# Optimization experiments

Hardware: AMD Instinct MI355X
Metric: run time of the kernel (lower is better)

Reference implementation:

```python
import jax, jax.numpy as jnp
import numpy as np

B, S, HID, H = 4, 2048, 768, 12
D = HID // H  # 64
SCALE = 1.0 / (D ** 0.5)


def setup_inputs() -> dict:
    key = jax.random.key(0)
    ks = jax.random.split(key, 12)
    std = 0.02
    inp = {
        'Q': jax.random.normal(ks[0], (B, S, HID), jnp.float32),
        'K': jax.random.normal(ks[1], (B, S, HID), jnp.float32),
        'V': jax.random.normal(ks[2], (B, S, HID), jnp.float32),
        'attn_mask': jax.random.randint(ks[3], (B, S, S), 0, 2) == 1,
        'Wq': jax.random.normal(ks[4], (HID, HID), jnp.float32) * std,
        'bq': jnp.zeros((HID,), jnp.float32),
        'Wk': jax.random.normal(ks[5], (HID, HID), jnp.float32) * std,
        'bk': jnp.zeros((HID,), jnp.float32),
        'Wv': jax.random.normal(ks[6], (HID, HID), jnp.float32) * std,
        'bv': jnp.zeros((HID,), jnp.float32),
        'Wo': jax.random.normal(ks[7], (HID, HID), jnp.float32) * std,
        'bo': jnp.zeros((HID,), jnp.float32),
    }
    return inp


def reference(Q, K, V, attn_mask, Wq, bq, Wk, bk, Wv, bv, Wo, bo):
    b, s, _ = Q.shape
    # projections -> [b, h, s, d]
    def split_heads(x):
        return x.reshape(b, s, H, D).transpose(0, 2, 1, 3)
    q = split_heads(Q @ Wq + bq)
    k = split_heads(K @ Wk + bk)
    v = split_heads(V @ Wv + bv)
    # eager attention: materialize full [b,h,s,s] scores
    scores = jnp.einsum('bhqd,bhkd->bhqk', q, k) * SCALE
    scores = jnp.where(attn_mask[:, None, :, :], jnp.float32(-1e9), scores)
    attn_prob = jax.nn.softmax(scores, axis=-1)
    # dropout is identity in eval mode
    context = jnp.einsum('bhqk,bhkd->bhqd', attn_prob, v)
    context = context.transpose(0, 2, 1, 3).reshape(b, s, H * D)
    output = context @ Wo + bo
    return (output, attn_prob)
```

## Files before the change

kernel.cpp:

```cpp
#include <hip/hip_runtime.h>
#include <hip/hip_bf16.h>
#include <stdint.h>

#define BB 4
#define SS 2048
#define HIDD 768
#define HH 12
#define DD 64
#define SCALE_F 0.125f

using bf16 = __hip_bfloat16;
typedef __attribute__((ext_vector_type(8))) short short8v;
typedef __attribute__((ext_vector_type(4))) float f32x4;

__device__ __forceinline__ float ldf(const float* p, size_t i) { return p[i]; }
__device__ __forceinline__ float ldf(const bf16* p, size_t i) { return __bfloat162float(p[i]); }
__device__ __forceinline__ void stf(float* p, size_t i, float v) { p[i] = v; }
__device__ __forceinline__ void stf(bf16* p, size_t i, float v) { p[i] = __float2bfloat16(v); }

__device__ __forceinline__ uint32_t bfb(float f) {
    bf16 h = __float2bfloat16(f);
    uint16_t u;
    __builtin_memcpy(&u, &h, 2);
    return (uint32_t)u;
}
__device__ __forceinline__ float b2f(uint32_t u) {
    uint32_t w = u << 16;
    float f;
    __builtin_memcpy(&f, &w, 4);
    return f;
}

__device__ __forceinline__ uint4 load8p(const bf16* p) { return *(const uint4*)p; }
__device__ __forceinline__ uint4 load8p(const float* p) {
    float4 a = *(const float4*)p;
    float4 b = *(const float4*)(p + 4);
    uint4 r;
    r.x = bfb(a.x) | (bfb(a.y) << 16);
    r.y = bfb(a.z) | (bfb(a.w) << 16);
    r.z = bfb(b.x) | (bfb(b.y) << 16);
    r.w = bfb(b.z) | (bfb(b.w) << 16);
    return r;
}

template <int ITERS, typename TIN>
__device__ __forceinline__ void stage_tile(char* dst, const TIN* src, int rowStride, int tid) {
    #pragma unroll
    for (int i = 0; i < ITERS; i++) {
        int u = tid + (i << 8);
        int r = u >> 3, sg = u & 7;
        uint4 v = load8p(src + (size_t)r * rowStride + sg * 8);
        *(uint4*)(dst + r * 128 + ((sg * 16) ^ ((r & 7) << 4))) = v;
    }
}

__device__ __forceinline__ short8v ldfrag(const char* base, int row, int bofs) {
    return *(const short8v*)(base + row * 128 + (bofs ^ ((row & 7) << 4)));
}

__global__ void detect_kernel(const uint32_t* __restrict__ qraw,
                              const uint32_t* __restrict__ mraw,
                              int* __restrict__ flags) {
    __shared__ int ci, cn;
    int tid = threadIdx.x;
    if (tid == 0) { ci = 0; cn = 0; }
    __syncthreads();
    int li = 0;
    for (int l = 0; l < 8; l++) {
        uint32_t w = qraw[tid + l * 256];
        #pragma unroll
        for (int h = 0; h < 2; h++) {
            uint32_t bits = (h ? (w >> 16) : (w & 0xffffu)) << 16;
            float f = __uint_as_float(bits);
            float a = fabsf(f);
            if (a != 0.0f && (a > 1e3f || a < 1e-4f)) li++;
        }
    }
    int ln = 0;
    for (int l = 0; l < 4; l++) {
        if (mraw[tid + l * 256] > 1u) ln++;
    }
    atomicAdd(&ci, li);
    atomicAdd(&cn, ln);
    __syncthreads();
    if (tid == 0) {
        flags[0] = (ci > 1024) ? 0 : 1;
        flags[1] = (cn > 64) ? 1 : 0;
    }
}

__global__ __launch_bounds__(256) void bitpack_mask(const int* __restrict__ flags,
                                                    const void* __restrict__ maskp,
                                                    uint64_t* __restrict__ mbits) {
    int gw = (int)((blockIdx.x * 256 + threadIdx.x) >> 6);
    int lane = threadIdx.x & 63;
    int byteM = flags[1];
    const int* mi = (const int*)maskp;
    const uint8_t* mb = (const uint8_t*)maskp;
    for (int it = 0; it < 64; it++) {
        size_t wi = (size_t)gw * 64 + it;
        size_t e = wi * 64 + lane;
        int m = byteM ? (int)mb[e] : mi[e];
        unsigned long long b = __ballot(m != 0);
        if (lane == 0) mbits[wi] = (uint64_t)b;
    }
}

template <typename T>
__global__ __launch_bounds__(256) void transpose_w(const int* __restrict__ flags, int want,
                                                   const T* __restrict__ W0,
                                                   const T* __restrict__ W1,
                                                   const T* __restrict__ W2,
                                                   const T* __restrict__ W3,
                                                   bf16* __restrict__ WT) {
    if (flags[0] != want) return;
    __shared__ uint16_t tb[64][65];
    int tid = threadIdx.x;
    int z = blockIdx.z;
    const T* W = (z == 0) ? W0 : (z == 1) ? W1 : (z == 2) ? W2 : W3;
    int k0 = blockIdx.y * 64, n0 = blockIdx.x * 64;
    #pragma unroll
    for (int l = 0; l < 16; l++) {
        int idx = tid + l * 256;
        int r = idx >> 6, c = idx & 63;
        tb[c][r] = (uint16_t)bfb(ldf(W, (size_t)(k0 + r) * HIDD + n0 + c));
    }
    __syncthreads();
    bf16* dst = WT + (size_t)z * HIDD * HIDD;
    #pragma unroll
    for (int l = 0; l < 16; l++) {
        int idx = tid + l * 256;
        int r = idx >> 6, c = idx & 63;
        *(uint16_t*)&dst[(size_t)(n0 + r) * HIDD + k0 + c] = tb[r][c];
    }
}

template <typename TX, typename TO, int HSPLIT>
__global__ __launch_bounds__(256) void gemm2(const int* __restrict__ flags, int want,
                                             const TX* __restrict__ X,
                                             const bf16* __restrict__ WT,
                                             const TO* __restrict__ bias,
                                             bf16* __restrict__ Yh,
                                             TO* __restrict__ Yl) {
    if (flags[0] != want) return;
    __shared__ char xs[128 * 128];
    __shared__ char ws[64 * 128];
    int tid = threadIdx.x;
    int lane = tid & 63, w = tid >> 6;
    int g = lane >> 4, t = lane & 15;
    int row0 = blockIdx.y * 128, n0 = blockIdx.x * 64;
    const f32x4 fz = {0.f, 0.f, 0.f, 0.f};
    f32x4 acc[2][4];
    #pragma unroll
    for (int rb = 0; rb < 2; rb++)
        #pragma unroll
        for (int c = 0; c < 4; c++) acc[rb][c] = fz;
    for (int kt = 0; kt < HIDD; kt += 64) {
        stage_tile<4>(xs, X + (size_t)row0 * HIDD + kt, HIDD, tid);
        stage_tile<2>(ws, WT + (size_t)n0 * HIDD + kt, HIDD, tid);
        __syncthreads();
        #pragma unroll
        for (int ks = 0; ks < 2; ks++) {
            short8v a0 = ldfrag(xs, w * 32 + t, g * 16 + ks * 64);
            short8v a1 = ldfrag(xs, w * 32 + 16 + t, g * 16 + ks * 64);
            #pragma unroll
            for (int c = 0; c < 4; c++) {
                short8v b = ldfrag(ws, c * 16 + t, g * 16 + ks * 64);
                acc[0][c] = __builtin_amdgcn_mfma_f32_16x16x32_bf16(a0, b, acc[0][c], 0, 0, 0);
                acc[1][c] = __builtin_amdgcn_mfma_f32_16x16x32_bf16(a1, b, acc[1][c], 0, 0, 0);
            }
        }
        __syncthreads();
    }
    #pragma unroll
    for (int c = 0; c < 4; c++) {
        int col = n0 + c * 16 + t;
        float bv = ldf(bias, (size_t)col);
        #pragma unroll
        for (int rb = 0; rb < 2; rb++) {
            #pragma unroll
            for (int r = 0; r < 4; r++) {
                int row = row0 + w * 32 + rb * 16 + g * 4 + r;
                float v = acc[rb][c][r] + bv;
                if (HSPLIT) {
                    int b_ = row >> 11, s = row & 2047, h = col >> 6, d = col & 63;
                    Yh[(((size_t)b_ * HH + h) * SS + s) * DD + d] = __float2bfloat16(v);
                } else {
                    stf(Yl, (size_t)row * HIDD + col, v);
                }
            }
        }
    }
}

__global__ __launch_bounds__(256) void transpose_v(const bf16* __restrict__ vh,
                                                   bf16* __restrict__ vt) {
    __shared__ uint16_t tb[64][65];
    int tid = threadIdx.x;
    int s0 = blockIdx.x * 64, bh = blockIdx.y;
    const bf16* src = vh + ((size_t)bh * SS + s0) * DD;
    #pragma unroll
    for (int i = 0; i < 2; i++) {
        int u = tid + (i << 8);
        int r = u >> 3, sg = u & 7;
        uint4 v = *(const uint4*)(src + (size_t)r * DD + sg * 8);
        uint32_t wv[4] = {v.x, v.y, v.z, v.w};
        #pragma unroll
        for (int j = 0; j < 4; j++) {
            tb[r][sg * 8 + 2 * j]     = (uint16_t)(wv[j] & 0xffffu);
            tb[r][sg * 8 + 2 * j + 1] = (uint16_t)(wv[j] >> 16);
        }
    }
    __syncthreads();
    bf16* dst = vt + (size_t)bh * DD * SS + s0;
    #pragma unroll
    for (int i = 0; i < 2; i++) {
        int u = tid + (i << 8);
        int d = u >> 3, sg = u & 7;
        uint32_t w0 = (uint32_t)tb[sg * 8 + 0][d] | ((uint32_t)tb[sg * 8 + 1][d] << 16);
        uint32_t w1 = (uint32_t)tb[sg * 8 + 2][d] | ((uint32_t)tb[sg * 8 + 3][d] << 16);
        uint32_t w2 = (uint32_t)tb[sg * 8 + 4][d] | ((uint32_t)tb[sg * 8 + 5][d] << 16);
        uint32_t w3 = (uint32_t)tb[sg * 8 + 6][d] | ((uint32_t)tb[sg * 8 + 7][d] << 16);
        uint4 o; o.x = w0; o.y = w1; o.z = w2; o.w = w3;
        *(uint4*)(dst + (size_t)d * SS + sg * 8) = o;
    }
}

template <typename T>
__global__ __launch_bounds__(256) void fused_attn2(const int* __restrict__ flags, int want,
                                                   const bf16* __restrict__ qh,
                                                   const bf16* __restrict__ kh,
                                                   const bf16* __restrict__ vt,
                                                   const uint64_t* __restrict__ mbits,
                                                   T* __restrict__ P,
                                                   bf16* __restrict__ ctx) {
    if (flags[0] != want) return;
    __shared__ char pl[16 * 4096];
    __shared__ char st[64 * 128];
    __shared__ float red[4][16];
    __shared__ float invl[16];
    int tid = threadIdx.x;
    int lane = tid & 63, w = tid >> 6;
    int g = lane >> 4, t = lane & 15;
    int q0 = blockIdx.x * 16, bh = blockIdx.y;
    int b_ = bh / HH, h = bh - b_ * HH;
    const f32x4 fz = {0.f, 0.f, 0.f, 0.f};

    const bf16* qbase = qh + ((size_t)bh * SS + q0 + t) * DD;
    short8v aq[2];
    aq[0] = *(const short8v*)(qbase + g * 8);
    aq[1] = *(const short8v*)(qbase + 32 + g * 8);

    const bf16* kbh = kh + (size_t)bh * SS * DD;
    const bf16* vbh = vt + (size_t)bh * DD * SS;
    size_t mrow[4];
    #pragma unroll
    for (int r = 0; r < 4; r++) mrow[r] = ((size_t)b_ * SS + q0 + g * 4 + r) * (SS / 64);

    float sum4[4] = {0.f, 0.f, 0.f, 0.f};
    int bitIdx = w * 16 + t;

    for (int kt = 0; kt < SS; kt += 64) {
        stage_tile<2>(st, kbh + (size_t)kt * DD, DD, tid);
        __syncthreads();
        f32x4 s = fz;
        #pragma unroll
        for (int ks = 0; ks < 2; ks++) {
            short8v b = ldfrag(st, w * 16 + t, g * 16 + ks * 64);
            s = __builtin_amdgcn_mfma_f32_16x16x32_bf16(aq[ks], b, s, 0, 0, 0);
        }
        #pragma unroll
        for (int r = 0; r < 4; r++) {
            uint64_t mw = mbits[mrow[r] + (kt >> 6)];
            int msk = (int)((mw >> bitIdx) & 1ull);
            float sv = msk ? -1e30f : s[r] * SCALE_F;
            float p = __expf(fminf(sv, 30.0f));
            sum4[r] += p;
            int row = g * 4 + r;
            int colb = (kt + w * 16 + t) * 2;
            *(uint16_t*)(pl + row * 4096 + (colb ^ ((row & 7) << 4))) = (uint16_t)bfb(p);
        }
        __syncthreads();
    }
    #pragma unroll
    for (int r = 0; r < 4; r++) {
        float v = sum4[r];
        #pragma unroll
        for (int d = 1; d < 16; d <<= 1) v += __shfl_xor(v, d);
        if (t == 0) red[w][g * 4 + r] = v;
    }
    __syncthreads();
    if (tid < 16) {
        float tot = red[0][tid] + red[1][tid] + red[2][tid] + red[3][tid];
        invl[tid] = (tot > 0.f) ? 1.0f / tot : 0.0f;
    }
    __syncthreads();
    float invr[4];
    #pragma unroll
    for (int r = 0; r < 4; r++) invr[r] = invl[g * 4 + r];
    int prow = tid >> 4;
    float pinv = invl[prow];
    T* Prow = P + ((size_t)bh * SS + q0 + prow) * SS;

    f32x4 o = fz;
    for (int kt = 0; kt < SS; kt += 64) {
        stage_tile<2>(st, vbh + kt, SS, tid);
        __syncthreads();
        #pragma unroll
        for (int ks = 0; ks < 2; ks++) {
            short8v ap = *(const short8v*)(pl + t * 4096 +
                            (((kt + ks * 32 + g * 8) * 2) ^ ((t & 7) << 4)));
            short8v bv = ldfrag(st, w * 16 + t, g * 16 + ks * 64);
            o = __builtin_amdgcn_mfma_f32_16x16x32_bf16(ap, bv, o, 0, 0, 0);
        }
        {
            int col = kt + (tid & 15) * 4;
            uint2 pv2 = *(const uint2*)(pl + prow * 4096 + ((col * 2) ^ ((prow & 7) << 4)));
            float p0 = b2f(pv2.x & 0xffffu) * pinv;
            float p1 = b2f(pv2.x >> 16) * pinv;
            float p2 = b2f(pv2.y & 0xffffu) * pinv;
            float p3 = b2f(pv2.y >> 16) * pinv;
            stf(Prow, (size_t)col + 0, p0);
            stf(Prow, (size_t)col + 1, p1);
            stf(Prow, (size_t)col + 2, p2);
            stf(Prow, (size_t)col + 3, p3);
        }
        __syncthreads();
    }
    #pragma unroll
    for (int r = 0; r < 4; r++) {
        int q = q0 + g * 4 + r;
        ctx[((size_t)b_ * SS + q) * HIDD + h * DD + w * 16 + t] =
            __float2bfloat16(o[r] * invr[r]);
    }
}

extern "C" void kernel_launch(void* const* d_in, const int* in_sizes, int n_in,
                              void* d_out, int out_size, void* d_ws, size_t ws_size,
                              hipStream_t stream) {
    const size_t nqkv = (size_t)BB * SS * HIDD;
    const size_t nw = (size_t)HIDD * HIDD;
    const size_t nmw = (size_t)BB * SS * (SS / 64);

    bf16* qh = (bf16*)d_ws;
    bf16* kh = qh + nqkv;
    bf16* vh = kh + nqkv;
    bf16* vt = vh + nqkv;
    bf16* WT = vt + nqkv;
    uint64_t* mbits = (uint64_t*)(WT + 4 * nw);
    int* flags = (int*)(mbits + nmw);
    bf16* ctx = vh;

    detect_kernel<<<1, 256, 0, stream>>>((const uint32_t*)d_in[0], (const uint32_t*)d_in[3], flags);
    bitpack_mask<<<1024, 256, 0, stream>>>(flags, d_in[3], mbits);

    dim3 blk(256);
    dim3 gW(HIDD / 64, HIDD / 64, 4);
    dim3 gG(HIDD / 64, (BB * SS) / 128);
    dim3 gT(SS / 64, BB * HH);
    dim3 gF(SS / 16, BB * HH);

    transpose_w<float><<<gW, blk, 0, stream>>>(flags, 0,
        (const float*)d_in[4], (const float*)d_in[6], (const float*)d_in[8],
        (const float*)d_in[10], WT);
    transpose_w<bf16><<<gW, blk, 0, stream>>>(flags, 1,
        (const bf16*)d_in[4], (const bf16*)d_in[6], (const bf16*)d_in[8],
        (const bf16*)d_in[10], WT);

    {
        gemm2<float, float, 1><<<gG, blk, 0, stream>>>(flags, 0, (const float*)d_in[0],
            WT + 0 * nw, (const float*)d_in[5], qh, (float*)nullptr);
        gemm2<float, float, 1><<<gG, blk, 0, stream>>>(flags, 0, (const float*)d_in[1],
            WT + 1 * nw, (const float*)d_in[7], kh, (float*)nullptr);
        gemm2<float, float, 1><<<gG, blk, 0, stream>>>(flags, 0, (const float*)d_in[2],
            WT + 2 * nw, (const float*)d_in[9], vh, (float*)nullptr);
        gemm2<bf16, bf16, 1><<<gG, blk, 0, stream>>>(flags, 1, (const bf16*)d_in[0],
            WT + 0 * nw, (const bf16*)d_in[5], qh, (bf16*)nullptr);
        gemm2<bf16, bf16, 1><<<gG, blk, 0, stream>>>(flags, 1, (const bf16*)d_in[1],
            WT + 1 * nw, (const bf16*)d_in[7], kh, (bf16*)nullptr);
        gemm2<bf16, bf16, 1><<<gG, blk, 0, stream>>>(flags, 1, (const bf16*)d_in[2],
            WT + 2 * nw, (const bf16*)d_in[9], vh, (bf16*)nullptr);
    }

    transpose_v<<<gT, blk, 0, stream>>>(vh, vt);

    {
        float* out = (float*)d_out;
        float* P = out + nqkv;
        fused_attn2<float><<<gF, blk, 0, stream>>>(flags, 0, qh, kh, vt, mbits, P, ctx);
    }
    {
        bf16* out = (bf16*)d_out;
        bf16* P = out + nqkv;
        fused_attn2<bf16><<<gF, blk, 0, stream>>>(flags, 1, qh, kh, vt, mbits, P, ctx);
    }

    {
        float* out = (float*)d_out;
        gemm2<bf16, float, 0><<<gG, blk, 0, stream>>>(flags, 0, ctx, WT + 3 * nw,
            (const float*)d_in[11], (bf16*)nullptr, out);
    }
    {
        bf16* out = (bf16*)d_out;
        gemm2<bf16, bf16, 0><<<gG, blk, 0, stream>>>(flags, 1, ctx, WT + 3 * nw,
            (const bf16*)d_in[11], (bf16*)nullptr, out);
    }
}
```

Before: 1.705 ms.

## Restructure attention to single pass with register-prefetched K/V and direct-to-LDS GEMM loads

The fused attention kernel now computes scores and P·V in one loop, reading K and V fragments straight from global memory into registers with one-tile-ahead prefetch. This removes the separate K/V LDS staging passes and most barriers. The probability matrix is written at the end with wide non-temporal stores. Inputs and biases are pre-converted to bf16 and f32 in staging kernels (using the P output region as scratch), and the GEMM uses global_load_lds to copy tiles directly into LDS. Duplicate flag-gated launches are collapsed into one runtime-branching kernel each, at the cost of extra conversion passes and reuse of output memory as temporary space.

```diff
diff --git a/kernel.cpp b/kernel.cpp
--- a/kernel.cpp
+++ b/kernel.cpp
@@ -8,15 +8,18 @@
 #define HH 12
 #define DD 64
 #define SCALE_F 0.125f
+#define NQKV ((size_t)BB * SS * HIDD)
+#define NW ((size_t)HIDD * HIDD)
+#define NMW ((size_t)BB * SS * (SS / 64))
 
 using bf16 = __hip_bfloat16;
 typedef __attribute__((ext_vector_type(8))) short short8v;
 typedef __attribute__((ext_vector_type(4))) float f32x4;
+typedef __attribute__((ext_vector_type(4))) float fvec4;
+typedef __attribute__((ext_vector_type(4))) unsigned int uvec4;
 
 __device__ __forceinline__ float ldf(const float* p, size_t i) { return p[i]; }
 __device__ __forceinline__ float ldf(const bf16* p, size_t i) { return __bfloat162float(p[i]); }
-__device__ __forceinline__ void stf(float* p, size_t i, float v) { p[i] = v; }
-__device__ __forceinline__ void stf(bf16* p, size_t i, float v) { p[i] = __float2bfloat16(v); }
 
 __device__ __forceinline__ uint32_t bfb(float f) {
     bf16 h = __float2bfloat16(f);
@@ -30,8 +33,6 @@
     __builtin_memcpy(&f, &w, 4);
     return f;
 }
-
-__device__ __forceinline__ uint4 load8p(const bf16* p) { return *(const uint4*)p; }
 __device__ __forceinline__ uint4 load8p(const float* p) {
     float4 a = *(const float4*)p;
     float4 b = *(const float4*)(p + 4);
@@ -43,19 +44,14 @@
     return r;
 }
 
-template <int ITERS, typename TIN>
-__device__ __forceinline__ void stage_tile(char* dst, const TIN* src, int rowStride, int tid) {
-    #pragma unroll
-    for (int i = 0; i < ITERS; i++) {
-        int u = tid + (i << 8);
-        int r = u >> 3, sg = u & 7;
-        uint4 v = load8p(src + (size_t)r * rowStride + sg * 8);
-        *(uint4*)(dst + r * 128 + ((sg * 16) ^ ((r & 7) << 4))) = v;
-    }
-}
-
 __device__ __forceinline__ short8v ldfrag(const char* base, int row, int bofs) {
     return *(const short8v*)(base + row * 128 + (bofs ^ ((row & 7) << 4)));
+}
+
+typedef __attribute__((address_space(1))) void as1_void;
+typedef __attribute__((address_space(3))) void as3_void;
+__device__ __forceinline__ void gload16(const void* g, void* l) {
+    __builtin_amdgcn_global_load_lds((as1_void*)g, (as3_void*)l, 16, 0, 0);
 }
 
 __global__ void detect_kernel(const uint32_t* __restrict__ qraw,
@@ -106,27 +102,56 @@
     }
 }
 
-template <typename T>
-__global__ __launch_bounds__(256) void transpose_w(const int* __restrict__ flags, int want,
-                                                   const T* __restrict__ W0,
-                                                   const T* __restrict__ W1,
-                                                   const T* __restrict__ W2,
-                                                   const T* __restrict__ W3,
-                                                   bf16* __restrict__ WT) {
-    if (flags[0] != want) return;
+__global__ __launch_bounds__(256) void convert_in(const int* __restrict__ flags,
+                                                  const void* __restrict__ Q,
+                                                  const void* __restrict__ K,
+                                                  const void* __restrict__ V,
+                                                  bf16* __restrict__ xb) {
+    int isbf = flags[0];
+    int z = blockIdx.y;
+    const void* src = (z == 0) ? Q : (z == 1) ? K : V;
+    size_t base = ((size_t)blockIdx.x * 256 + threadIdx.x) * 8;
+    bf16* dst = xb + (size_t)z * NQKV + base;
+    if (isbf) {
+        *(uint4*)dst = *(const uint4*)((const bf16*)src + base);
+    } else {
+        *(uint4*)dst = load8p((const float*)src + base);
+    }
+}
+
+__global__ void convert_bias(const int* __restrict__ flags,
+                             const void* __restrict__ b0, const void* __restrict__ b1,
+                             const void* __restrict__ b2, const void* __restrict__ b3,
+                             float* __restrict__ bf) {
+    int isbf = flags[0];
+    for (int i = threadIdx.x; i < 4 * HIDD; i += 256) {
+        int z = i / HIDD, j = i - z * HIDD;
+        const void* b = (z == 0) ? b0 : (z == 1) ? b1 : (z == 2) ? b2 : b3;
+        bf[i] = isbf ? b2f((uint32_t) * ((const uint16_t*)b + j)) : ((const float*)b)[j];
+    }
+}
+
+__global__ __launch_bounds__(256) void transpose_w2(const int* __restrict__ flags,
+                                                    const void* __restrict__ W0,
+                                                    const void* __restrict__ W1,
+                                                    const void* __restrict__ W2,
+                                                    const void* __restrict__ W3,
+                                                    bf16* __restrict__ WT) {
+    int isbf = flags[0];
     __shared__ uint16_t tb[64][65];
     int tid = threadIdx.x;
     int z = blockIdx.z;
-    const T* W = (z == 0) ? W0 : (z == 1) ? W1 : (z == 2) ? W2 : W3;
+    const void* W = (z == 0) ? W0 : (z == 1) ? W1 : (z == 2) ? W2 : W3;
     int k0 = blockIdx.y * 64, n0 = blockIdx.x * 64;
     #pragma unroll
     for (int l = 0; l < 16; l++) {
         int idx = tid + l * 256;
         int r = idx >> 6, c = idx & 63;
-        tb[c][r] = (uint16_t)bfb(ldf(W, (size_t)(k0 + r) * HIDD + n0 + c));
-    }
-    __syncthreads();
-    bf16* dst = WT + (size_t)z * HIDD * HIDD;
+        size_t off = (size_t)(k0 + r) * HIDD + n0 + c;
+        tb[c][r] = isbf ? *((const uint16_t*)W + off) : (uint16_t)bfb(((const float*)W)[off]);
+    }
+    __syncthreads();
+    bf16* dst = WT + (size_t)z * NW;
     #pragma unroll
     for (int l = 0; l < 16; l++) {
         int idx = tid + l * 256;
@@ -135,14 +160,14 @@
     }
 }
 
-template <typename TX, typename TO, int HSPLIT>
-__global__ __launch_bounds__(256) void gemm2(const int* __restrict__ flags, int want,
-                                             const TX* __restrict__ X,
+template <int HSPLIT>
+__global__ __launch_bounds__(256) void gemm3(const int* __restrict__ flags,
+                                             const bf16* __restrict__ X,
                                              const bf16* __restrict__ WT,
-                                             const TO* __restrict__ bias,
+                                             const float* __restrict__ biasf,
                                              bf16* __restrict__ Yh,
-                                             TO* __restrict__ Yl) {
-    if (flags[0] != want) return;
+                                             float* __restrict__ Yf,
+                                             bf16* __restrict__ Yb) {
     __shared__ char xs[128 * 128];
     __shared__ char ws[64 * 128];
     int tid = threadIdx.x;
@@ -155,9 +180,22 @@
     for (int rb = 0; rb < 2; rb++)
         #pragma unroll
         for (int c = 0; c < 4; c++) acc[rb][c] = fz;
+    int r8 = tid >> 3, c8 = tid & 7;
+    const char* Xb0 = (const char*)(X + (size_t)row0 * HIDD);
+    const char* Wb0 = (const char*)(WT + (size_t)n0 * HIDD);
     for (int kt = 0; kt < HIDD; kt += 64) {
-        stage_tile<4>(xs, X + (size_t)row0 * HIDD + kt, HIDD, tid);
-        stage_tile<2>(ws, WT + (size_t)n0 * HIDD + kt, HIDD, tid);
+        #pragma unroll
+        for (int i = 0; i < 4; i++) {
+            int r = r8 + i * 32;
+            gload16(Xb0 + (size_t)r * (HIDD * 2) + kt * 2 + ((c8 * 16) ^ ((r & 7) << 4)),
+                    xs + w * 1024 + i * 4096);
+        }
+        #pragma unroll
+        for (int i = 0; i < 2; i++) {
+            int r = r8 + i * 32;
+            gload16(Wb0 + (size_t)r * (HIDD * 2) + kt * 2 + ((c8 * 16) ^ ((r & 7) << 4)),
+                    ws + w * 1024 + i * 4096);
+        }
         __syncthreads();
         #pragma unroll
         for (int ks = 0; ks < 2; ks++) {
@@ -172,10 +210,11 @@
         }
         __syncthreads();
     }
+    int isbf = flags[0];
     #pragma unroll
     for (int c = 0; c < 4; c++) {
         int col = n0 + c * 16 + t;
-        float bv = ldf(bias, (size_t)col);
+        float bv = biasf[col];
         #pragma unroll
         for (int rb = 0; rb < 2; rb++) {
             #pragma unroll
@@ -183,10 +222,11 @@
                 int row = row0 + w * 32 + rb * 16 + g * 4 + r;
                 float v = acc[rb][c][r] + bv;
                 if (HSPLIT) {
-                    int b_ = row >> 11, s = row & 2047, h = col >> 6, d = col & 63;
-                    Yh[(((size_t)b_ * HH + h) * SS + s) * DD + d] = __float2bfloat16(v);
+                    int b_ = row >> 11, s = row & 2047, h2 = col >> 6, d = col & 63;
+                    Yh[(((size_t)b_ * HH + h2) * SS + s) * DD + d] = __float2bfloat16(v);
                 } else {
-                    stf(Yl, (size_t)row * HIDD + col, v);
+                    if (isbf) Yb[(size_t)row * HIDD + col] = __float2bfloat16(v);
+                    else      Yf[(size_t)row * HIDD + col] = v;
                 }
             }
         }
@@ -226,17 +266,16 @@
     }
 }
 
-template <typename T>
-__global__ __launch_bounds__(256) void fused_attn2(const int* __restrict__ flags, int want,
+__global__ __launch_bounds__(256) void fused_attn3(const int* __restrict__ flags,
                                                    const bf16* __restrict__ qh,
                                                    const bf16* __restrict__ kh,
                                                    const bf16* __restrict__ vt,
                                                    const uint64_t* __restrict__ mbits,
-                                                   T* __restrict__ P,
+                                                   float* __restrict__ Pf,
+                                                   bf16* __restrict__ Ph,
                                                    bf16* __restrict__ ctx) {
-    if (flags[0] != want) return;
+    const int isf32 = (flags[0] == 0);
     __shared__ char pl[16 * 4096];
-    __shared__ char st[64 * 128];
     __shared__ float red[4][16];
     __shared__ float invl[16];
     int tid = threadIdx.x;
@@ -245,43 +284,73 @@
     int q0 = blockIdx.x * 16, bh = blockIdx.y;
     int b_ = bh / HH, h = bh - b_ * HH;
     const f32x4 fz = {0.f, 0.f, 0.f, 0.f};
+    int bitIdx = w * 16 + t;
 
     const bf16* qbase = qh + ((size_t)bh * SS + q0 + t) * DD;
-    short8v aq[2];
-    aq[0] = *(const short8v*)(qbase + g * 8);
-    aq[1] = *(const short8v*)(qbase + 32 + g * 8);
-
-    const bf16* kbh = kh + (size_t)bh * SS * DD;
-    const bf16* vbh = vt + (size_t)bh * DD * SS;
-    size_t mrow[4];
-    #pragma unroll
-    for (int r = 0; r < 4; r++) mrow[r] = ((size_t)b_ * SS + q0 + g * 4 + r) * (SS / 64);
+    short8v aq0 = *(const short8v*)(qbase + g * 8);
+    short8v aq1 = *(const short8v*)(qbase + 32 + g * 8);
+
+    const bf16* kcol = kh + ((size_t)bh * SS + bitIdx) * DD + g * 8;
+    const bf16* vrow = vt + ((size_t)bh * DD + bitIdx) * SS + g * 8;
+    const uint64_t* mrowp[4];
+    #pragma unroll
+    for (int r = 0; r < 4; r++)
+        mrowp[r] = mbits + ((size_t)b_ * SS + q0 + g * 4 + r) * (SS / 64);
+
+    short8v cK0 = *(const short8v*)(kcol);
+    short8v cK1 = *(const short8v*)(kcol + 32);
+    short8v cV0 = *(const short8v*)(vrow);
+    short8v cV1 = *(const short8v*)(vrow + 32);
+    uint64_t cM[4];
+    #pragma unroll
+    for (int r = 0; r < 4; r++) cM[r] = mrowp[r][0];
 
     float sum4[4] = {0.f, 0.f, 0.f, 0.f};
-    int bitIdx = w * 16 + t;
+    f32x4 o = fz;
 
     for (int kt = 0; kt < SS; kt += 64) {
-        stage_tile<2>(st, kbh + (size_t)kt * DD, DD, tid);
-        __syncthreads();
+        int ktn = (kt + 64) & (SS - 1);
+        const bf16* kn = kcol + (size_t)ktn * DD;
+        const bf16* vn = vrow + ktn;
+        short8v nK0 = *(const short8v*)(kn);
+        short8v nK1 = *(const short8v*)(kn + 32);
+        short8v nV0 = *(const short8v*)(vn);
+        short8v nV1 = *(const short8v*)(vn + 32);
+        int wn = ((kt >> 6) + 1) & 31;
+        uint64_t nM[4];
+        #pragma unroll
+        for (int r = 0; r < 4; r++) nM[r] = mrowp[r][wn];
+
         f32x4 s = fz;
-        #pragma unroll
-        for (int ks = 0; ks < 2; ks++) {
-            short8v b = ldfrag(st, w * 16 + t, g * 16 + ks * 64);
-            s = __builtin_amdgcn_mfma_f32_16x16x32_bf16(aq[ks], b, s, 0, 0, 0);
-        }
+        s = __builtin_amdgcn_mfma_f32_16x16x32_bf16(aq0, cK0, s, 0, 0, 0);
+        s = __builtin_amdgcn_mfma_f32_16x16x32_bf16(aq1, cK1, s, 0, 0, 0);
+
         #pragma unroll
         for (int r = 0; r < 4; r++) {
-            uint64_t mw = mbits[mrow[r] + (kt >> 6)];
-            int msk = (int)((mw >> bitIdx) & 1ull);
+            int msk = (int)((cM[r] >> bitIdx) & 1ull);
             float sv = msk ? -1e30f : s[r] * SCALE_F;
             float p = __expf(fminf(sv, 30.0f));
             sum4[r] += p;
             int row = g * 4 + r;
-            int colb = (kt + w * 16 + t) * 2;
+            int colb = (kt + bitIdx) * 2;
             *(uint16_t*)(pl + row * 4096 + (colb ^ ((row & 7) << 4))) = (uint16_t)bfb(p);
         }
-        __syncthreads();
-    }
+
+        asm volatile("s_waitcnt lgkmcnt(0)" ::: "memory");
+        __builtin_amdgcn_s_barrier();
+        asm volatile("" ::: "memory");
+        __builtin_amdgcn_sched_barrier(0);
+
+        short8v ap0 = *(const short8v*)(pl + t * 4096 + (((kt + g * 8) * 2) ^ ((t & 7) << 4)));
+        short8v ap1 = *(const short8v*)(pl + t * 4096 + (((kt + 32 + g * 8) * 2) ^ ((t & 7) << 4)));
+        o = __builtin_amdgcn_mfma_f32_16x16x32_bf16(ap0, cV0, o, 0, 0, 0);
+        o = __builtin_amdgcn_mfma_f32_16x16x32_bf16(ap1, cV1, o, 0, 0, 0);
+
+        cK0 = nK0; cK1 = nK1; cV0 = nV0; cV1 = nV1;
+        #pragma unroll
+        for (int r = 0; r < 4; r++) cM[r] = nM[r];
+    }
+
     #pragma unroll
     for (int r = 0; r < 4; r++) {
         float v = sum4[r];
@@ -295,114 +364,83 @@
         invl[tid] = (tot > 0.f) ? 1.0f / tot : 0.0f;
     }
     __syncthreads();
-    float invr[4];
-    #pragma unroll
-    for (int r = 0; r < 4; r++) invr[r] = invl[g * 4 + r];
-    int prow = tid >> 4;
-    float pinv = invl[prow];
-    T* Prow = P + ((size_t)bh * SS + q0 + prow) * SS;
-
-    f32x4 o = fz;
-    for (int kt = 0; kt < SS; kt += 64) {
-        stage_tile<2>(st, vbh + kt, SS, tid);
-        __syncthreads();
-        #pragma unroll
-        for (int ks = 0; ks < 2; ks++) {
-            short8v ap = *(const short8v*)(pl + t * 4096 +
-                            (((kt + ks * 32 + g * 8) * 2) ^ ((t & 7) << 4)));
-            short8v bv = ldfrag(st, w * 16 + t, g * 16 + ks * 64);
-            o = __builtin_amdgcn_mfma_f32_16x16x32_bf16(ap, bv, o, 0, 0, 0);
-        }
-        {
-            int col = kt + (tid & 15) * 4;
-            uint2 pv2 = *(const uint2*)(pl + prow * 4096 + ((col * 2) ^ ((prow & 7) << 4)));
-            float p0 = b2f(pv2.x & 0xffffu) * pinv;
-            float p1 = b2f(pv2.x >> 16) * pinv;
-            float p2 = b2f(pv2.y & 0xffffu) * pinv;
-            float p3 = b2f(pv2.y >> 16) * pinv;
-            stf(Prow, (size_t)col + 0, p0);
-            stf(Prow, (size_t)col + 1, p1);
-            stf(Prow, (size_t)col + 2, p2);
-            stf(Prow, (size_t)col + 3, p3);
-        }
-        __syncthreads();
-    }
+
     #pragma unroll
     for (int r = 0; r < 4; r++) {
         int q = q0 + g * 4 + r;
-        ctx[((size_t)b_ * SS + q) * HIDD + h * DD + w * 16 + t] =
-            __float2bfloat16(o[r] * invr[r]);
+        ctx[((size_t)b_ * SS + q) * HIDD + h * DD + bitIdx] =
+            __float2bfloat16(o[r] * invl[g * 4 + r]);
+    }
+
+    int prow = tid >> 4, cg = tid & 15;
+    float pinv = invl[prow];
+    size_t rowb = ((size_t)bh * SS + q0 + prow) * SS;
+    if (isf32) {
+        #pragma unroll
+        for (int c0 = 0; c0 < SS; c0 += 128) {
+            int col = c0 + cg * 8;
+            uint4 pv = *(const uint4*)(pl + prow * 4096 + ((col * 2) ^ ((prow & 7) << 4)));
+            fvec4 lo = {b2f(pv.x & 0xffffu) * pinv, b2f(pv.x >> 16) * pinv,
+                        b2f(pv.y & 0xffffu) * pinv, b2f(pv.y >> 16) * pinv};
+            fvec4 hi = {b2f(pv.z & 0xffffu) * pinv, b2f(pv.z >> 16) * pinv,
+                        b2f(pv.w & 0xffffu) * pinv, b2f(pv.w >> 16) * pinv};
+            __builtin_nontemporal_store(lo, (fvec4*)(Pf + rowb + col));
+            __builtin_nontemporal_store(hi, (fvec4*)(Pf + rowb + col + 4));
+        }
+    } else {
+        #pragma unroll
+        for (int c0 = 0; c0 < SS; c0 += 128) {
+            int col = c0 + cg * 8;
+            uint4 pv = *(const uint4*)(pl + prow * 4096 + ((col * 2) ^ ((prow & 7) << 4)));
+            uvec4 ov;
+            ov.x = bfb(b2f(pv.x & 0xffffu) * pinv) | (bfb(b2f(pv.x >> 16) * pinv) << 16);
+            ov.y = bfb(b2f(pv.y & 0xffffu) * pinv) | (bfb(b2f(pv.y >> 16) * pinv) << 16);
+            ov.z = bfb(b2f(pv.z & 0xffffu) * pinv) | (bfb(b2f(pv.z >> 16) * pinv) << 16);
+            ov.w = bfb(b2f(pv.w & 0xffffu) * pinv) | (bfb(b2f(pv.w >> 16) * pinv) << 16);
+            __builtin_nontemporal_store(ov, (uvec4*)(Ph + rowb + col));
+        }
     }
 }
 
 extern "C" void kernel_launch(void* const* d_in, const int* in_sizes, int n_in,
                               void* d_out, int out_size, void* d_ws, size_t ws_size,
                               hipStream_t stream) {
-    const size_t nqkv = (size_t)BB * SS * HIDD;
-    const size_t nw = (size_t)HIDD * HIDD;
-    const size_t nmw = (size_t)BB * SS * (SS / 64);
-
     bf16* qh = (bf16*)d_ws;
-    bf16* kh = qh + nqkv;
-    bf16* vh = kh + nqkv;
-    bf16* vt = vh + nqkv;
-    bf16* WT = vt + nqkv;
-    uint64_t* mbits = (uint64_t*)(WT + 4 * nw);
-    int* flags = (int*)(mbits + nmw);
+    bf16* kh = qh + NQKV;
+    bf16* vh = kh + NQKV;
+    bf16* vt = vh + NQKV;
+    bf16* WT = vt + NQKV;
+    uint64_t* mbits = (uint64_t*)(WT + 4 * NW);
+    int* flags = (int*)(mbits + NMW);
+    float* bfp = (float*)(flags + 4);
     bf16* ctx = vh;
+
+    bf16* xb = (bf16*)((char*)d_out + NQKV * 4);
 
     detect_kernel<<<1, 256, 0, stream>>>((const uint32_t*)d_in[0], (const uint32_t*)d_in[3], flags);
     bitpack_mask<<<1024, 256, 0, stream>>>(flags, d_in[3], mbits);
+    convert_in<<<dim3(3072, 3), 256, 0, stream>>>(flags, d_in[0], d_in[1], d_in[2], xb);
+    convert_bias<<<1, 256, 0, stream>>>(flags, d_in[5], d_in[7], d_in[9], d_in[11], bfp);
+    transpose_w2<<<dim3(12, 12, 4), 256, 0, stream>>>(flags, d_in[4], d_in[6], d_in[8],
+                                                      d_in[10], WT);
 
     dim3 blk(256);
-    dim3 gW(HIDD / 64, HIDD / 64, 4);
     dim3 gG(HIDD / 64, (BB * SS) / 128);
     dim3 gT(SS / 64, BB * HH);
     dim3 gF(SS / 16, BB * HH);
 
-    transpose_w<float><<<gW, blk, 0, stream>>>(flags, 0,
-        (const float*)d_in[4], (const float*)d_in[6], (const float*)d_in[8],
-        (const float*)d_in[10], WT);
-    transpose_w<bf16><<<gW, blk, 0, stream>>>(flags, 1,
-        (const bf16*)d_in[4], (const bf16*)d_in[6], (const bf16*)d_in[8],
-        (const bf16*)d_in[10], WT);
-
-    {
-        gemm2<float, float, 1><<<gG, blk, 0, stream>>>(flags, 0, (const float*)d_in[0],
-            WT + 0 * nw, (const float*)d_in[5], qh, (float*)nullptr);
-        gemm2<float, float, 1><<<gG, blk, 0, stream>>>(flags, 0, (const float*)d_in[1],
-            WT + 1 * nw, (const float*)d_in[7], kh, (float*)nullptr);
-        gemm2<float, float, 1><<<gG, blk, 0, stream>>>(flags, 0, (const float*)d_in[2],
-            WT + 2 * nw, (const float*)d_in[9], vh, (float*)nullptr);
-        gemm2<bf16, bf16, 1><<<gG, blk, 0, stream>>>(flags, 1, (const bf16*)d_in[0],
-            WT + 0 * nw, (const bf16*)d_in[5], qh, (bf16*)nullptr);
-        gemm2<bf16, bf16, 1><<<gG, blk, 0, stream>>>(flags, 1, (const bf16*)d_in[1],
-            WT + 1 * nw, (const bf16*)d_in[7], kh, (bf16*)nullptr);
-        gemm2<bf16, bf16, 1><<<gG, blk, 0, stream>>>(flags, 1, (const bf16*)d_in[2],
-            WT + 2 * nw, (const bf16*)d_in[9], vh, (bf16*)nullptr);
-    }
+    gemm3<1><<<gG, blk, 0, stream>>>(flags, xb + 0 * NQKV, WT + 0 * NW, bfp + 0 * HIDD,
+                                     qh, nullptr, nullptr);
+    gemm3<1><<<gG, blk, 0, stream>>>(flags, xb + 1 * NQKV, WT + 1 * NW, bfp + 1 * HIDD,
+                                     kh, nullptr, nullptr);
+    gemm3<1><<<gG, blk, 0, stream>>>(flags, xb + 2 * NQKV, WT + 2 * NW, bfp + 2 * HIDD,
+                                     vh, nullptr, nullptr);
 
     transpose_v<<<gT, blk, 0, stream>>>(vh, vt);
 
-    {
-        float* out = (float*)d_out;
-        float* P = out + nqkv;
-        fused_attn2<float><<<gF, blk, 0, stream>>>(flags, 0, qh, kh, vt, mbits, P, ctx);
-    }
-    {
-        bf16* out = (bf16*)d_out;
-        bf16* P = out + nqkv;
-        fused_attn2<bf16><<<gF, blk, 0, stream>>>(flags, 1, qh, kh, vt, mbits, P, ctx);
-    }
-
-    {
-        float* out = (float*)d_out;
-        gemm2<bf16, float, 0><<<gG, blk, 0, stream>>>(flags, 0, ctx, WT + 3 * nw,
-            (const float*)d_in[11], (bf16*)nullptr, out);
-    }
-    {
-        bf16* out = (bf16*)d_out;
-        gemm2<bf16, bf16, 0><<<gG, blk, 0, stream>>>(flags, 1, ctx, WT + 3 * nw,
-            (const bf16*)d_in[11], (bf16*)nullptr, out);
-    }
-}
+    fused_attn3<<<gF, blk, 0, stream>>>(flags, qh, kh, vt, mbits,
+                                        (float*)d_out + NQKV, (bf16*)d_out + NQKV, ctx);
+
+    gemm3<0><<<gG, blk, 0, stream>>>(flags, ctx, WT + 3 * NW, bfp + 3 * HIDD,
+                                     nullptr, (float*)d_out, (bf16*)d_out);
+}
```

After: 1.466 ms. -14.1%, faster.
